# Performance work log

Measured on AMD Instinct MI355X. Metric: run time of the kernel, lower is better.

## Reference

```python
import jax, jax.numpy as jnp
import numpy as np

N_ITERS = 3   # Routing default n_iters
EPS = 1e-5    # variance floor added to sig2
LN_EPS = 1e-5 # torch LayerNorm eps


def _routing(a_inp, mu_inp, W, Bias, beta_use, beta_ign):
    """Heinsen routing (gaussian p_model).
    a_inp: [b, n_i]; mu_inp: [b, n_i, c, d_inp]
    W: [1 or n_i, n_o, d_inp, d_out]; Bias: [n_o, c, d_out]; betas: [n_o].
    """
    if W.shape[0] == 1:  # weights shared across input capsules (n_inp not fixed)
        V = jnp.einsum('jdh,bicd->bijch', W[0], mu_inp) + Bias
    else:
        V = jnp.einsum('ijdh,bicd->bijch', W, mu_inp) + Bias
    n_out = V.shape[2]
    fa = jax.nn.sigmoid(a_inp)[..., None]          # [b, n_i, 1]
    R = jnp.full(V.shape[:3], 1.0 / n_out, dtype=V.dtype)
    a_out = mu_out = sig2 = Vm2 = None
    for it in range(N_ITERS):
        # E-step
        if it > 0:
            log_p = (-jnp.einsum('bijch,bjch->bij', Vm2, 1.0 / (2.0 * sig2))
                     - 0.5 * jnp.log(sig2).sum(axis=(-2, -1))[:, None, :])
            R = jax.nn.softmax(jax.nn.log_sigmoid(a_out)[:, None, :] + log_p, axis=-1)
        # D-step
        D_use = fa * R                              # [b, n_i, n_o]
        D_sum = D_use.sum(axis=-2)                  # [b, n_o]
        # M-step
        a_out = beta_use * D_sum - beta_ign * (fa.sum(axis=-2) - D_sum)
        nR = D_use / D_sum[:, None, :]
        mu_out = jnp.einsum('bij,bijch->bjch', nR, V)
        Vm2 = jnp.square(V - mu_out[:, None])
        sig2 = jnp.einsum('bij,bijch->bjch', nR, Vm2) + EPS
    return a_out, mu_out, sig2


def setup_inputs() -> dict:
    B, T = 32, 128
    d_depth, d_emb, d_cap, n_parts, n_classes = 13, 1024, 16, 64, 5
    key = jax.random.key(0)
    ks = jax.random.split(key, 8)
    mask = jax.random.uniform(ks[0], (B, T), jnp.float32, 0.05, 0.95)  # in (0,1) so logit is finite
    embs = jax.random.normal(ks[1], (B, T, d_depth, d_emb), jnp.float32)
    depth_emb = jax.random.normal(ks[2], (d_depth, d_emb), jnp.float32) * 0.02
    ln_w = jnp.ones((d_emb,), jnp.float32)
    ln_b = jnp.zeros((d_emb,), jnp.float32)
    dp_w = jax.random.normal(ks[3], (n_parts, d_emb), jnp.float32) * np.sqrt(2.0 / d_emb)  # kaiming
    dp_b = jnp.zeros((n_parts,), jnp.float32)
    # Routing 1: d_cov=1, d_inp=n_parts, d_out=d_cap, n_out=n_parts, n_inp shared (-1)
    W1 = jax.random.normal(ks[4], (1, n_parts, n_parts, d_cap), jnp.float32) / n_parts
    B1 = jnp.zeros((n_parts, 1, d_cap), jnp.float32)
    bu1 = jnp.zeros((n_parts,), jnp.float32)
    bi1 = jnp.zeros((n_parts,), jnp.float32)
    # Routing 2: d_cov=1, d_inp=d_cap, d_out=d_cap, n_out=n_classes, n_inp=n_parts
    W2 = jax.random.normal(ks[5], (n_parts, n_classes, d_cap, d_cap), jnp.float32) / d_cap
    B2 = jnp.zeros((n_classes, 1, d_cap), jnp.float32)
    bu2 = jnp.zeros((n_classes,), jnp.float32)
    bi2 = jnp.zeros((n_classes,), jnp.float32)
    return dict(mask=mask, embs=embs, depth_emb=depth_emb, ln_w=ln_w, ln_b=ln_b,
                dp_w=dp_w, dp_b=dp_b, W1=W1, B1=B1, bu1=bu1, bi1=bi1,
                W2=W2, B2=B2, bu2=bu2, bi2=bi2)


def reference(mask, embs, depth_emb, ln_w, ln_b, dp_w, dp_b,
              W1, B1, bu1, bi1, W2, B2, bu2, bi2):
    B = mask.shape[0]
    d_depth = embs.shape[-2]
    # input activations: logit(mask), repeated over depth
    a = jnp.log(mask / (1.0 - mask))                       # [B, T]
    a = jnp.broadcast_to(a[..., None], a.shape + (d_depth,)).reshape(B, -1)  # [B, T*d_depth]
    # detect_parts: LayerNorm -> Linear -> Swish
    x = embs + depth_emb
    m = x.mean(axis=-1, keepdims=True)
    v = ((x - m) ** 2).mean(axis=-1, keepdims=True)        # biased var (torch LayerNorm)
    xn = (x - m) * jax.lax.rsqrt(v + LN_EPS) * ln_w + ln_b
    h = jnp.einsum('btde,pe->btdp', xn, dp_w) + dp_b
    mu = h * jax.nn.sigmoid(h)                             # Swish
    mu = mu.reshape(B, -1, 1, mu.shape[-1])                # [B, T*d_depth, 1, n_parts]
    a, mu, sig2 = _routing(a, mu, W1, B1, bu1, bi1)
    a, mu, sig2 = _routing(a, mu, W2, B2, bu2, bi2)
    return a, mu, sig2
```

## Files before the change

### kernel.cpp

```cpp
#include <hip/hip_runtime.h>
#include <hip/hip_bf16.h>

constexpr int BQ = 32;
constexpr int TT = 128;
constexpr int DD = 13;
constexpr int E  = 1024;
constexpr int P  = 64;
constexpr int C  = 16;
constexpr int NC = 5;
constexpr int NI = TT * DD;
constexpr int NROWS = BQ * NI;
constexpr int RB = 8;

__global__ void k_sumfa(const float* __restrict__ mask, float* __restrict__ sumfa)
{
    const int b = blockIdx.x, tid = threadIdx.x;
    float v = mask[b * TT + tid];
#pragma unroll
    for (int off = 32; off > 0; off >>= 1) v += __shfl_xor(v, off);
    __shared__ float p2[2];
    if ((tid & 63) == 0) p2[tid >> 6] = v;
    __syncthreads();
    if (tid == 0) sumfa[b] = (float)DD * (p2[0] + p2[1]);
}

__global__ void k1_parts_v(const float* __restrict__ embs, const float* __restrict__ depth_emb,
                           const float* __restrict__ ln_w, const float* __restrict__ ln_b,
                           const float* __restrict__ dp_w, const float* __restrict__ dp_b,
                           const float* __restrict__ W1,  const float* __restrict__ B1,
                           float* __restrict__ V)
{
    __shared__ float xn[RB][E];
    __shared__ float muL[RB][P];
    const int tid = threadIdx.x;
    const int wave = tid >> 6, lane = tid & 63;
    const int row0 = blockIdx.x * RB;

    for (int rr = 0; rr < 2; ++rr) {
        const int r = wave * 2 + rr;
        const int row = row0 + r;
        const int dd = row % DD;
        const float* xr = embs + (size_t)row * E;
        const float* de = depth_emb + (size_t)dd * E;
        float4 xv[4];
        float s = 0.f;
#pragma unroll
        for (int k = 0; k < 4; ++k) {
            const int e = 4 * lane + 256 * k;
            float4 a = *reinterpret_cast<const float4*>(xr + e);
            const float4 d4 = *reinterpret_cast<const float4*>(de + e);
            a.x += d4.x; a.y += d4.y; a.z += d4.z; a.w += d4.w;
            xv[k] = a;
            s += a.x + a.y + a.z + a.w;
        }
#pragma unroll
        for (int off = 32; off > 0; off >>= 1) s += __shfl_xor(s, off);
        const float mean = s * (1.f / E);
        float vs = 0.f;
#pragma unroll
        for (int k = 0; k < 4; ++k) {
            const float4 a = xv[k];
            const float dx = a.x - mean, dy = a.y - mean, dz = a.z - mean, dw = a.w - mean;
            vs += dx * dx + dy * dy + dz * dz + dw * dw;
        }
#pragma unroll
        for (int off = 32; off > 0; off >>= 1) vs += __shfl_xor(vs, off);
        const float rstd = rsqrtf(vs * (1.f / E) + 1e-5f);
#pragma unroll
        for (int k = 0; k < 4; ++k) {
            const int e = 4 * lane + 256 * k;
            const float4 a = xv[k];
            const float4 w4 = *reinterpret_cast<const float4*>(ln_w + e);
            const float4 b4 = *reinterpret_cast<const float4*>(ln_b + e);
            float4 o4;
            o4.x = (a.x - mean) * rstd * w4.x + b4.x;
            o4.y = (a.y - mean) * rstd * w4.y + b4.y;
            o4.z = (a.z - mean) * rstd * w4.z + b4.z;
            o4.w = (a.w - mean) * rstd * w4.w + b4.w;
            *reinterpret_cast<float4*>(&xn[r][e]) = o4;
        }
    }
    __syncthreads();

    {
        const int p = tid >> 2, eq = tid & 3;
        float hacc[RB];
#pragma unroll
        for (int r = 0; r < RB; ++r) hacc[r] = 0.f;
        const float* wp = dp_w + (size_t)p * E;
        for (int eb = 0; eb < E; eb += 16) {
            const float4 w4 = *reinterpret_cast<const float4*>(wp + eb + eq * 4);
#pragma unroll
            for (int r = 0; r < RB; ++r) {
                const float4 x4 = *reinterpret_cast<const float4*>(&xn[r][eb + eq * 4]);
                hacc[r] += w4.x * x4.x + w4.y * x4.y + w4.z * x4.z + w4.w * x4.w;
            }
        }
#pragma unroll
        for (int r = 0; r < RB; ++r) {
            float v = hacc[r];
            v += __shfl_xor(v, 1);
            v += __shfl_xor(v, 2);
            if (eq == 0) {
                const float h = v + dp_b[p];
                muL[r][p] = h / (1.f + __expf(-h));
            }
        }
    }
    __syncthreads();

    {
        const int j = tid >> 2, hq = tid & 3;
        float4 vacc[RB];
        const float4 b4 = *reinterpret_cast<const float4*>(B1 + j * C + hq * 4);
#pragma unroll
        for (int r = 0; r < RB; ++r) vacc[r] = b4;
        const float* w1p = W1 + ((size_t)j * P) * C + hq * 4;
        for (int d = 0; d < P; ++d) {
            const float4 w4 = *reinterpret_cast<const float4*>(w1p + (size_t)d * C);
#pragma unroll
            for (int r = 0; r < RB; ++r) {
                const float m = muL[r][d];
                vacc[r].x += m * w4.x; vacc[r].y += m * w4.y;
                vacc[r].z += m * w4.z; vacc[r].w += m * w4.w;
            }
        }
#pragma unroll
        for (int r = 0; r < RB; ++r) {
            const size_t row = (size_t)(row0 + r);
            *reinterpret_cast<float4*>(V + (row * P + j) * C + hq * 4) = vacc[r];
        }
    }
}

__global__ void k2_pass(const float* __restrict__ V, const float* __restrict__ mask,
                        const float* __restrict__ muo, const float* __restrict__ isg,
                        const float* __restrict__ biasv, float* __restrict__ Smu,
                        float* __restrict__ SV2, float* __restrict__ Dsum, const int it)
{
    __shared__ float lacc[P][34];
    const int tid = threadIdx.x;
    const int wave = tid >> 6, j = tid & 63;
    const int b = blockIdx.x / (NI / 64);
    const int tile = blockIdx.x % (NI / 64);

    for (int k = tid; k < P * 34; k += 256) (&lacc[0][0])[k] = 0.f;

    float mo[16], iv[16];
    float bj = 0.f;
    if (it > 0) {
        const float4* mp = reinterpret_cast<const float4*>(muo + ((size_t)b * P + j) * C);
        const float4* ip = reinterpret_cast<const float4*>(isg + ((size_t)b * P + j) * C);
#pragma unroll
        for (int k = 0; k < 4; ++k) {
            const float4 m4 = mp[k]; const float4 i4 = ip[k];
            mo[k * 4 + 0] = m4.x; mo[k * 4 + 1] = m4.y; mo[k * 4 + 2] = m4.z; mo[k * 4 + 3] = m4.w;
            iv[k * 4 + 0] = i4.x; iv[k * 4 + 1] = i4.y; iv[k * 4 + 2] = i4.z; iv[k * 4 + 3] = i4.w;
        }
        bj = biasv[(size_t)b * P + j];
    }

    float dsum = 0.f;
    float smuA[16], sv2A[16];
#pragma unroll
    for (int h = 0; h < 16; ++h) { smuA[h] = 0.f; sv2A[h] = 0.f; }

    __syncthreads();

    for (int s = 0; s < 16; ++s) {
        const int i = tile * 64 + wave * 16 + s;
        const float4* vp = reinterpret_cast<const float4*>(V + (((size_t)b * NI + i) * P + j) * C);
        float va[16];
        {
            const float4 t0 = vp[0], t1 = vp[1], t2 = vp[2], t3 = vp[3];
            va[0] = t0.x; va[1] = t0.y; va[2]  = t0.z; va[3]  = t0.w;
            va[4] = t1.x; va[5] = t1.y; va[6]  = t1.z; va[7]  = t1.w;
            va[8] = t2.x; va[9] = t2.y; va[10] = t2.z; va[11] = t2.w;
            va[12] = t3.x; va[13] = t3.y; va[14] = t3.z; va[15] = t3.w;
        }
        float R;
        if (it > 0) {
            float q = 0.f;
#pragma unroll
            for (int h = 0; h < 16; ++h) { const float d = va[h] - mo[h]; q += d * d * iv[h]; }
            const float sc = bj - q;
            float m = sc;
#pragma unroll
            for (int off = 32; off > 0; off >>= 1) m = fmaxf(m, __shfl_xor(m, off));
            const float e = __expf(sc - m);
            float sum = e;
#pragma unroll
            for (int off = 32; off > 0; off >>= 1) sum += __shfl_xor(sum, off);
            R = e / sum;
        } else {
            R = 1.f / 64.f;
        }
        const float fa = mask[b * TT + i / DD];
        const float w = fa * R;
        dsum += w;
#pragma unroll
        for (int h = 0; h < 16; ++h) {
            smuA[h] += w * va[h];
            sv2A[h] += w * va[h] * va[h];
        }
    }

#pragma unroll
    for (int h = 0; h < 16; ++h) {
        atomicAdd(&lacc[j][h], smuA[h]);
        atomicAdd(&lacc[j][16 + h], sv2A[h]);
    }
    atomicAdd(&lacc[j][32], dsum);
    __syncthreads();

    for (int k = tid; k < P * 33; k += 256) {
        const int jj = k / 33, r = k % 33;
        const float v = lacc[jj][r];
        if (r < 16)      atomicAdd(&Smu[((size_t)b * P + jj) * C + r], v);
        else if (r < 32) atomicAdd(&SV2[((size_t)b * P + jj) * C + (r - 16)], v);
        else             atomicAdd(&Dsum[(size_t)b * P + jj], v);
    }
}

__global__ void k2f(const float* __restrict__ Smu, const float* __restrict__ SV2,
                    const float* __restrict__ Dsum, const float* __restrict__ sumfa,
                    const float* __restrict__ bu, const float* __restrict__ bi,
                    float* __restrict__ muo, float* __restrict__ isg,
                    float* __restrict__ biasv, float* __restrict__ a1)
{
    const int t = blockIdx.x * blockDim.x + threadIdx.x;
    if (t >= BQ * P) return;
    const int b = t / P, j = t % P;
    const float ds = Dsum[t];
    const float inv = 1.f / ds;
    const float ao = bu[j] * ds - bi[j] * (sumfa[b] - ds);
    a1[t] = ao;
    const float lsg = (ao < 0.f) ? (ao - log1pf(__expf(ao))) : (-log1pf(__expf(-ao)));
    float sumlog = 0.f;
#pragma unroll
    for (int h = 0; h < C; ++h) {
        const float m = Smu[t * C + h] * inv;
        const float s2 = fmaxf(SV2[t * C + h] * inv - m * m, 0.f) + 1e-5f;
        muo[t * C + h] = m;
        isg[t * C + h] = 0.5f / s2;
        sumlog += logf(s2);
    }
    biasv[t] = lsg - 0.5f * sumlog;
}

__global__ void k3_routing2(const float* __restrict__ muo, const float* __restrict__ a1,
                            const float* __restrict__ W2, const float* __restrict__ B2,
                            const float* __restrict__ bu2, const float* __restrict__ bi2,
                            float* __restrict__ out)
{
    __shared__ float mu1L[P][C];
    __shared__ float faL[P];
    __shared__ float V2L[P][NC][C];
    __shared__ float RL[P][NC];
    __shared__ float mu2L[NC][C];
    __shared__ float s2L[NC][C];
    __shared__ float isL[NC][C];
    __shared__ float dsL[NC];
    __shared__ float biasL[NC];
    __shared__ float a2L[NC];
    __shared__ float sumfa2s;
    const int b = blockIdx.x, tid = threadIdx.x;

    for (int k = tid; k < P * C; k += 256) (&mu1L[0][0])[k] = muo[(size_t)b * P * C + k];
    if (tid < P) {
        const float a = a1[(size_t)b * P + tid];
        faL[tid] = 1.f / (1.f + __expf(-a));
    }
    __syncthreads();
    if (tid == 0) {
        float s = 0.f;
        for (int i = 0; i < P; ++i) s += faL[i];
        sumfa2s = s;
    }
    {
        const int i = tid >> 2, hq = tid & 3;
        for (int jj = 0; jj < NC; ++jj) {
            float4 acc = *reinterpret_cast<const float4*>(B2 + jj * C + hq * 4);
            const float* wp = W2 + ((size_t)(i * NC + jj) * C) * C + hq * 4;
#pragma unroll
            for (int d = 0; d < C; ++d) {
                const float m = mu1L[i][d];
                const float4 w4 = *reinterpret_cast<const float4*>(wp + d * C);
                acc.x += m * w4.x; acc.y += m * w4.y; acc.z += m * w4.z; acc.w += m * w4.w;
            }
            *reinterpret_cast<float4*>(&V2L[i][jj][hq * 4]) = acc;
        }
    }
    __syncthreads();

    for (int it = 0; it < 3; ++it) {
        if (tid < P) {
            const int i = tid;
            if (it == 0) {
#pragma unroll
                for (int jj = 0; jj < NC; ++jj) RL[i][jj] = 1.f / NC;
            } else {
                float sc[NC];
                float m = -3.4e38f;
#pragma unroll
                for (int jj = 0; jj < NC; ++jj) {
                    float q = 0.f;
#pragma unroll
                    for (int h = 0; h < C; ++h) {
                        const float d = V2L[i][jj][h] - mu2L[jj][h];
                        q += d * d * isL[jj][h];
                    }
                    sc[jj] = biasL[jj] - q;
                    m = fmaxf(m, sc[jj]);
                }
                float sum = 0.f;
#pragma unroll
                for (int jj = 0; jj < NC; ++jj) { sc[jj] = __expf(sc[jj] - m); sum += sc[jj]; }
                const float invs = 1.f / sum;
#pragma unroll
                for (int jj = 0; jj < NC; ++jj) RL[i][jj] = sc[jj] * invs;
            }
        }
        __syncthreads();
        if (tid < NC) {
            float ds = 0.f;
            for (int i = 0; i < P; ++i) ds += faL[i] * RL[i][tid];
            dsL[tid] = ds;
        }
        __syncthreads();
        if (tid < NC * C) {
            const int jj = tid / C, h = tid % C;
            float smu = 0.f, sv2 = 0.f;
            for (int i = 0; i < P; ++i) {
                const float w = faL[i] * RL[i][jj];
                const float v = V2L[i][jj][h];
                smu += w * v;
                sv2 += w * v * v;
            }
            const float inv = 1.f / dsL[jj];
            const float m = smu * inv;
            const float s2 = fmaxf(sv2 * inv - m * m, 0.f) + 1e-5f;
            mu2L[jj][h] = m;
            s2L[jj][h] = s2;
            isL[jj][h] = 0.5f / s2;
        }
        __syncthreads();
        if (tid < NC) {
            const float ds = dsL[tid];
            const float ao = bu2[tid] * ds - bi2[tid] * (sumfa2s - ds);
            a2L[tid] = ao;
            const float lsg = (ao < 0.f) ? (ao - log1pf(__expf(ao))) : (-log1pf(__expf(-ao)));
            float sl = 0.f;
#pragma unroll
            for (int h = 0; h < C; ++h) sl += logf(s2L[tid][h]);
            biasL[tid] = lsg - 0.5f * sl;
        }
        __syncthreads();
    }

    if (tid < NC) out[(size_t)b * NC + tid] = a2L[tid];
    if (tid < NC * C) {
        const int jj = tid / C, h = tid % C;
        out[BQ * NC + ((size_t)b * NC + jj) * C + h] = mu2L[jj][h];
        out[BQ * NC + BQ * NC * C + ((size_t)b * NC + jj) * C + h] = s2L[jj][h];
    }
}

extern "C" void kernel_launch(void* const* d_in, const int* in_sizes, int n_in,
                              void* d_out, int out_size, void* d_ws, size_t ws_size,
                              hipStream_t stream)
{
    (void)in_sizes; (void)n_in; (void)out_size; (void)ws_size;
    const float* mask      = (const float*)d_in[0];
    const float* embs      = (const float*)d_in[1];
    const float* depth_emb = (const float*)d_in[2];
    const float* ln_w      = (const float*)d_in[3];
    const float* ln_b      = (const float*)d_in[4];
    const float* dp_w      = (const float*)d_in[5];
    const float* dp_b      = (const float*)d_in[6];
    const float* W1        = (const float*)d_in[7];
    const float* B1        = (const float*)d_in[8];
    const float* bu1       = (const float*)d_in[9];
    const float* bi1       = (const float*)d_in[10];
    const float* W2        = (const float*)d_in[11];
    const float* B2        = (const float*)d_in[12];
    const float* bu2       = (const float*)d_in[13];
    const float* bi2       = (const float*)d_in[14];
    float* out = (float*)d_out;

    float* ws = (float*)d_ws;
    size_t o = 0;
    float* V     = ws + o; o += (size_t)NROWS * P * C;
    float* Smu   = ws + o; o += (size_t)BQ * P * C;
    float* SV2   = ws + o; o += (size_t)BQ * P * C;
    float* Dsum  = ws + o; o += (size_t)BQ * P;
    float* muo   = ws + o; o += (size_t)BQ * P * C;
    float* isg   = ws + o; o += (size_t)BQ * P * C;
    float* biasv = ws + o; o += (size_t)BQ * P;
    float* a1    = ws + o; o += (size_t)BQ * P;
    float* sumfa = ws + o; o += (size_t)BQ;

    k_sumfa<<<BQ, 128, 0, stream>>>(mask, sumfa);
    k1_parts_v<<<NROWS / RB, 256, 0, stream>>>(embs, depth_emb, ln_w, ln_b,
                                               dp_w, dp_b, W1, B1, V);
    for (int it = 0; it < 3; ++it) {
        hipMemsetAsync(Smu, 0, (size_t)(2 * BQ * P * C + BQ * P) * sizeof(float), stream);
        k2_pass<<<BQ * (NI / 64), 256, 0, stream>>>(V, mask, muo, isg, biasv,
                                                    Smu, SV2, Dsum, it);
        k2f<<<(BQ * P) / 256, 256, 0, stream>>>(Smu, SV2, Dsum, sumfa, bu1, bi1,
                                                muo, isg, biasv, a1);
    }
    k3_routing2<<<BQ, 256, 0, stream>>>(muo, a1, W2, B2, bu2, bi2, out);
}
```

Before: 880.6 us.

## Transpose V layout, register-tile part projection, expand quadratic form in routing pass

V is now stored as [row][h][j] so lanes indexed by output capsule j read coalesced scalars in the routing pass, and that pass double-buffers the next input's V values in registers. The part-detection kernel doubles rows per block and register-tiles four parts per thread over 16-lane groups to cut shared-memory reads per FMA. The routing E-step's (v-mu)^2*iv term is expanded into precomputed c0/c1 coefficients so each element needs two FMAs. These changes raise register pressure, and the expanded quadratic form can lose precision through cancellation.

After: 931.4 us. 1.06x slower.

```diff
diff --git a/kernel.cpp b/kernel.cpp
--- a/kernel.cpp
+++ b/kernel.cpp
@@ -10,7 +10,7 @@
 constexpr int NC = 5;
 constexpr int NI = TT * DD;
 constexpr int NROWS = BQ * NI;
-constexpr int RB = 8;
+constexpr int RB = 16;
 
 __global__ void k_sumfa(const float* __restrict__ mask, float* __restrict__ sumfa)
 {
@@ -24,11 +24,12 @@
     if (tid == 0) sumfa[b] = (float)DD * (p2[0] + p2[1]);
 }
 
-__global__ void k1_parts_v(const float* __restrict__ embs, const float* __restrict__ depth_emb,
-                           const float* __restrict__ ln_w, const float* __restrict__ ln_b,
-                           const float* __restrict__ dp_w, const float* __restrict__ dp_b,
-                           const float* __restrict__ W1,  const float* __restrict__ B1,
-                           float* __restrict__ V)
+__global__ __launch_bounds__(256) void
+k1_parts_v(const float* __restrict__ embs, const float* __restrict__ depth_emb,
+           const float* __restrict__ ln_w, const float* __restrict__ ln_b,
+           const float* __restrict__ dp_w, const float* __restrict__ dp_b,
+           const float* __restrict__ W1,  const float* __restrict__ B1,
+           float* __restrict__ V)
 {
     __shared__ float xn[RB][E];
     __shared__ float muL[RB][P];
@@ -36,8 +37,8 @@
     const int wave = tid >> 6, lane = tid & 63;
     const int row0 = blockIdx.x * RB;
 
-    for (int rr = 0; rr < 2; ++rr) {
-        const int r = wave * 2 + rr;
+    for (int rr = 0; rr < 4; ++rr) {
+        const int r = wave * 4 + rr;
         const int row = row0 + r;
         const int dd = row % DD;
         const float* xr = embs + (size_t)row * E;
@@ -83,60 +84,93 @@
     __syncthreads();
 
     {
-        const int p = tid >> 2, eq = tid & 3;
-        float hacc[RB];
-#pragma unroll
-        for (int r = 0; r < RB; ++r) hacc[r] = 0.f;
-        const float* wp = dp_w + (size_t)p * E;
-        for (int eb = 0; eb < E; eb += 16) {
-            const float4 w4 = *reinterpret_cast<const float4*>(wp + eb + eq * 4);
+        const int pg = tid >> 4, eq = tid & 15;
+        float acc[4][RB];
+#pragma unroll
+        for (int q = 0; q < 4; ++q)
+#pragma unroll
+            for (int r = 0; r < RB; ++r) acc[q][r] = 0.f;
+
+        for (int kk = 0; kk < 16; ++kk) {
+            const int e = kk * 64 + eq * 4;
+            float4 w4[4];
+#pragma unroll
+            for (int q = 0; q < 4; ++q)
+                w4[q] = *reinterpret_cast<const float4*>(dp_w + (size_t)(pg + q * 16) * E + e);
 #pragma unroll
             for (int r = 0; r < RB; ++r) {
-                const float4 x4 = *reinterpret_cast<const float4*>(&xn[r][eb + eq * 4]);
-                hacc[r] += w4.x * x4.x + w4.y * x4.y + w4.z * x4.z + w4.w * x4.w;
-            }
-        }
-#pragma unroll
-        for (int r = 0; r < RB; ++r) {
-            float v = hacc[r];
-            v += __shfl_xor(v, 1);
-            v += __shfl_xor(v, 2);
-            if (eq == 0) {
-                const float h = v + dp_b[p];
-                muL[r][p] = h / (1.f + __expf(-h));
+                const float4 x4 = *reinterpret_cast<const float4*>(&xn[r][e]);
+#pragma unroll
+                for (int q = 0; q < 4; ++q) {
+                    acc[q][r] = fmaf(w4[q].x, x4.x, acc[q][r]);
+                    acc[q][r] = fmaf(w4[q].y, x4.y, acc[q][r]);
+                    acc[q][r] = fmaf(w4[q].z, x4.z, acc[q][r]);
+                    acc[q][r] = fmaf(w4[q].w, x4.w, acc[q][r]);
+                }
+            }
+        }
+#pragma unroll
+        for (int q = 0; q < 4; ++q)
+#pragma unroll
+            for (int r = 0; r < RB; ++r) {
+                float v = acc[q][r];
+                v += __shfl_xor(v, 1);
+                v += __shfl_xor(v, 2);
+                v += __shfl_xor(v, 4);
+                v += __shfl_xor(v, 8);
+                acc[q][r] = v;
+            }
+        if (eq == 0) {
+#pragma unroll
+            for (int q = 0; q < 4; ++q) {
+                const int p = pg + q * 16;
+                const float bb = dp_b[p];
+#pragma unroll
+                for (int r = 0; r < RB; ++r) {
+                    const float h = acc[q][r] + bb;
+                    muL[r][p] = h / (1.f + __expf(-h));
+                }
             }
         }
     }
     __syncthreads();
 
     {
-        const int j = tid >> 2, hq = tid & 3;
-        float4 vacc[RB];
-        const float4 b4 = *reinterpret_cast<const float4*>(B1 + j * C + hq * 4);
-#pragma unroll
-        for (int r = 0; r < RB; ++r) vacc[r] = b4;
-        const float* w1p = W1 + ((size_t)j * P) * C + hq * 4;
+        const int h0 = wave * 4;
+        const int j = lane;
+        float4 acc[RB];
+        const float4 b4 = *reinterpret_cast<const float4*>(B1 + j * C + h0);
+#pragma unroll
+        for (int r = 0; r < RB; ++r) acc[r] = b4;
+        const float* w1p = W1 + (size_t)j * P * C + h0;
         for (int d = 0; d < P; ++d) {
             const float4 w4 = *reinterpret_cast<const float4*>(w1p + (size_t)d * C);
 #pragma unroll
             for (int r = 0; r < RB; ++r) {
                 const float m = muL[r][d];
-                vacc[r].x += m * w4.x; vacc[r].y += m * w4.y;
-                vacc[r].z += m * w4.z; vacc[r].w += m * w4.w;
+                acc[r].x = fmaf(m, w4.x, acc[r].x);
+                acc[r].y = fmaf(m, w4.y, acc[r].y);
+                acc[r].z = fmaf(m, w4.z, acc[r].z);
+                acc[r].w = fmaf(m, w4.w, acc[r].w);
             }
         }
 #pragma unroll
         for (int r = 0; r < RB; ++r) {
             const size_t row = (size_t)(row0 + r);
-            *reinterpret_cast<float4*>(V + (row * P + j) * C + hq * 4) = vacc[r];
-        }
-    }
-}
-
-__global__ void k2_pass(const float* __restrict__ V, const float* __restrict__ mask,
-                        const float* __restrict__ muo, const float* __restrict__ isg,
-                        const float* __restrict__ biasv, float* __restrict__ Smu,
-                        float* __restrict__ SV2, float* __restrict__ Dsum, const int it)
+            float* vp = V + (row * C + h0) * (size_t)P + j;
+            vp[0 * P] = acc[r].x;
+            vp[1 * P] = acc[r].y;
+            vp[2 * P] = acc[r].z;
+            vp[3 * P] = acc[r].w;
+        }
+    }
+}
+
+__global__ __launch_bounds__(256) void
+k2_pass(const float* __restrict__ V, const float* __restrict__ mask,
+        const float* __restrict__ c1v, const float* __restrict__ ivv,
+        const float* __restrict__ c0v, float* __restrict__ Smu,
+        float* __restrict__ SV2, float* __restrict__ Dsum, const int it)
 {
     __shared__ float lacc[P][34];
     const int tid = threadIdx.x;
@@ -146,19 +180,21 @@
 
     for (int k = tid; k < P * 34; k += 256) (&lacc[0][0])[k] = 0.f;
 
-    float mo[16], iv[16];
-    float bj = 0.f;
+    float c1[16], iv[16], c0 = 0.f;
     if (it > 0) {
-        const float4* mp = reinterpret_cast<const float4*>(muo + ((size_t)b * P + j) * C);
-        const float4* ip = reinterpret_cast<const float4*>(isg + ((size_t)b * P + j) * C);
+        const float4* cp = reinterpret_cast<const float4*>(c1v + ((size_t)b * P + j) * C);
+        const float4* ip = reinterpret_cast<const float4*>(ivv + ((size_t)b * P + j) * C);
 #pragma unroll
         for (int k = 0; k < 4; ++k) {
-            const float4 m4 = mp[k]; const float4 i4 = ip[k];
-            mo[k * 4 + 0] = m4.x; mo[k * 4 + 1] = m4.y; mo[k * 4 + 2] = m4.z; mo[k * 4 + 3] = m4.w;
+            const float4 c4 = cp[k]; const float4 i4 = ip[k];
+            c1[k * 4 + 0] = c4.x; c1[k * 4 + 1] = c4.y; c1[k * 4 + 2] = c4.z; c1[k * 4 + 3] = c4.w;
             iv[k * 4 + 0] = i4.x; iv[k * 4 + 1] = i4.y; iv[k * 4 + 2] = i4.z; iv[k * 4 + 3] = i4.w;
         }
-        bj = biasv[(size_t)b * P + j];
-    }
+        c0 = c0v[(size_t)b * P + j];
+    }
+
+    const int i0 = tile * 64 + wave * 16;
+    const float* vb = V + ((size_t)(b * NI + i0) * C) * P + j;
 
     float dsum = 0.f;
     float smuA[16], sv2A[16];
@@ -167,27 +203,30 @@
 
     __syncthreads();
 
+    float va[2][16];
+#pragma unroll
+    for (int h = 0; h < 16; ++h) va[0][h] = vb[(size_t)h * P];
+
+#pragma unroll
     for (int s = 0; s < 16; ++s) {
-        const int i = tile * 64 + wave * 16 + s;
-        const float4* vp = reinterpret_cast<const float4*>(V + (((size_t)b * NI + i) * P + j) * C);
-        float va[16];
-        {
-            const float4 t0 = vp[0], t1 = vp[1], t2 = vp[2], t3 = vp[3];
-            va[0] = t0.x; va[1] = t0.y; va[2]  = t0.z; va[3]  = t0.w;
-            va[4] = t1.x; va[5] = t1.y; va[6]  = t1.z; va[7]  = t1.w;
-            va[8] = t2.x; va[9] = t2.y; va[10] = t2.z; va[11] = t2.w;
-            va[12] = t3.x; va[13] = t3.y; va[14] = t3.z; va[15] = t3.w;
+        const int cb = s & 1;
+        if (s < 15) {
+#pragma unroll
+            for (int h = 0; h < 16; ++h)
+                va[cb ^ 1][h] = vb[(size_t)((s + 1) * C + h) * P];
         }
         float R;
         if (it > 0) {
-            float q = 0.f;
-#pragma unroll
-            for (int h = 0; h < 16; ++h) { const float d = va[h] - mo[h]; q += d * d * iv[h]; }
-            const float sc = bj - q;
-            float m = sc;
+            float q = c0;
+#pragma unroll
+            for (int h = 0; h < 16; ++h) {
+                const float v = va[cb][h];
+                q = fmaf(v, fmaf(-v, iv[h], c1[h]), q);
+            }
+            float m = q;
 #pragma unroll
             for (int off = 32; off > 0; off >>= 1) m = fmaxf(m, __shfl_xor(m, off));
-            const float e = __expf(sc - m);
+            const float e = __expf(q - m);
             float sum = e;
 #pragma unroll
             for (int off = 32; off > 0; off >>= 1) sum += __shfl_xor(sum, off);
@@ -195,13 +234,15 @@
         } else {
             R = 1.f / 64.f;
         }
+        const int i = i0 + s;
         const float fa = mask[b * TT + i / DD];
         const float w = fa * R;
         dsum += w;
 #pragma unroll
         for (int h = 0; h < 16; ++h) {
-            smuA[h] += w * va[h];
-            sv2A[h] += w * va[h] * va[h];
+            const float v = va[cb][h];
+            smuA[h] = fmaf(w, v, smuA[h]);
+            sv2A[h] = fmaf(w * v, v, sv2A[h]);
         }
     }
 
@@ -225,8 +266,9 @@
 __global__ void k2f(const float* __restrict__ Smu, const float* __restrict__ SV2,
                     const float* __restrict__ Dsum, const float* __restrict__ sumfa,
                     const float* __restrict__ bu, const float* __restrict__ bi,
-                    float* __restrict__ muo, float* __restrict__ isg,
-                    float* __restrict__ biasv, float* __restrict__ a1)
+                    float* __restrict__ muo, float* __restrict__ ivv,
+                    float* __restrict__ c1v, float* __restrict__ c0v,
+                    float* __restrict__ a1)
 {
     const int t = blockIdx.x * blockDim.x + threadIdx.x;
     if (t >= BQ * P) return;
@@ -236,16 +278,19 @@
     const float ao = bu[j] * ds - bi[j] * (sumfa[b] - ds);
     a1[t] = ao;
     const float lsg = (ao < 0.f) ? (ao - log1pf(__expf(ao))) : (-log1pf(__expf(-ao)));
-    float sumlog = 0.f;
+    float sumlog = 0.f, moiv = 0.f;
 #pragma unroll
     for (int h = 0; h < C; ++h) {
         const float m = Smu[t * C + h] * inv;
         const float s2 = fmaxf(SV2[t * C + h] * inv - m * m, 0.f) + 1e-5f;
+        const float iv = 0.5f / s2;
         muo[t * C + h] = m;
-        isg[t * C + h] = 0.5f / s2;
+        ivv[t * C + h] = iv;
+        c1v[t * C + h] = 2.f * m * iv;
         sumlog += logf(s2);
-    }
-    biasv[t] = lsg - 0.5f * sumlog;
+        moiv += m * m * iv;
+    }
+    c0v[t] = lsg - 0.5f * sumlog - moiv;
 }
 
 __global__ void k3_routing2(const float* __restrict__ muo, const float* __restrict__ a1,
@@ -395,8 +440,9 @@
     float* SV2   = ws + o; o += (size_t)BQ * P * C;
     float* Dsum  = ws + o; o += (size_t)BQ * P;
     float* muo   = ws + o; o += (size_t)BQ * P * C;
-    float* isg   = ws + o; o += (size_t)BQ * P * C;
-    float* biasv = ws + o; o += (size_t)BQ * P;
+    float* ivv   = ws + o; o += (size_t)BQ * P * C;
+    float* c1v   = ws + o; o += (size_t)BQ * P * C;
+    float* c0v   = ws + o; o += (size_t)BQ * P;
     float* a1    = ws + o; o += (size_t)BQ * P;
     float* sumfa = ws + o; o += (size_t)BQ;
 
@@ -405,10 +451,10 @@
                                                dp_w, dp_b, W1, B1, V);
     for (int it = 0; it < 3; ++it) {
         hipMemsetAsync(Smu, 0, (size_t)(2 * BQ * P * C + BQ * P) * sizeof(float), stream);
-        k2_pass<<<BQ * (NI / 64), 256, 0, stream>>>(V, mask, muo, isg, biasv,
+        k2_pass<<<BQ * (NI / 64), 256, 0, stream>>>(V, mask, c1v, ivv, c0v,
                                                     Smu, SV2, Dsum, it);
         k2f<<<(BQ * P) / 256, 256, 0, stream>>>(Smu, SV2, Dsum, sumfa, bu1, bi1,
-                                                muo, isg, biasv, a1);
+                                                muo, ivv, c1v, c0v, a1);
     }
     k3_routing2<<<BQ, 256, 0, stream>>>(muo, a1, W2, B2, bu2, bi2, out);
 }
```
